# Kernel tuning notes

Measured on AMD Instinct MI355X. Metric: run time of the kernel, lower is better.

The kernel has to match this reference:

```python
import jax, jax.numpy as jnp
import numpy as np

N, C, F = 16384, 8, 257
EPS = 1e-6
DELTA_MAX = 1e8


def setup_inputs() -> dict:
    key = jax.random.key(0)
    k1, k2, k3 = jax.random.split(key, 3)
    xr = jax.random.normal(k1, (N, C, F), dtype=jnp.float32)
    xi = jax.random.normal(k2, (N, C, F), dtype=jnp.float32)
    # affine params (reset_parameters: Wrr=Wii=1, Wri~U(-0.9,0.9), Br=Bi=0)
    Wrr = jnp.ones((C, F), dtype=jnp.float32)
    Wri = jax.random.uniform(k3, (C, F), dtype=jnp.float32, minval=-0.9, maxval=0.9)
    Wii = jnp.ones((C, F), dtype=jnp.float32)
    Br = jnp.zeros((C, F), dtype=jnp.float32)
    Bi = jnp.zeros((C, F), dtype=jnp.float32)
    return {"xr": xr, "xi": xi, "Wrr": Wrr, "Wri": Wri, "Wii": Wii, "Br": Br, "Bi": Bi}


def reference(xr, xi, Wrr, Wri, Wii, Br, Bi):
    # batch (training-mode) complex batchnorm over dim 0; stats per (channel, feature)
    Mr = jnp.mean(xr, axis=0, keepdims=True)  # [1,C,F]
    Mi = jnp.mean(xi, axis=0, keepdims=True)
    xr = xr - Mr
    xi = xi - Mi
    Vrr = jnp.mean(xr * xr, axis=0, keepdims=True)  # [1,C,F]
    Vri = jnp.mean(xr * xi, axis=0, keepdims=True)
    Vii = jnp.mean(xi * xi, axis=0, keepdims=True)
    tau = Vrr + Vii
    delta = jnp.clip(Vrr * Vii - Vri * Vri, EPS, DELTA_MAX)
    s = jnp.sqrt(delta)
    t = jnp.sqrt(tau + 2.0 * s)
    rst = 1.0 / (s * t)
    # inverse matrix square root of 2x2 covariance
    Urr = (s + Vii) * rst
    Uii = (s + Vrr) * rst
    Uri = -Vri * rst
    # affine mixing: Z = W @ U  (W, B broadcast [C,F] against [1,C,F])
    Zrr = Wrr * Urr + Wri * Uri
    Zri = Wrr * Uri + Wri * Uii
    Zir = Wri * Urr + Wii * Uri
    Zii = Wri * Uri + Wii * Uii
    yr = Zrr * xr + Zri * xi + Br
    yi = Zir * xr + Zii * xi + Bi
    return (yr, yi)
```

## Files before the change

kernel.cpp:

```cpp
#include <hip/hip_runtime.h>
#include <hip/hip_bf16.h>
#include <stdint.h>

#define NROWS   16384
#define NCOLS   2056
#define NG      257
#define EPSV    1e-6f
#define DELTA_MAX 1e8f

__device__ __forceinline__ float bf_lo(uint32_t u) {
    return __builtin_bit_cast(float, u << 16);
}
__device__ __forceinline__ float bf_hi(uint32_t u) {
    return __builtin_bit_cast(float, u & 0xffff0000u);
}
__device__ __forceinline__ float bf1(uint16_t u) {
    return __builtin_bit_cast(float, (uint32_t)u << 16);
}
__device__ __forceinline__ uint32_t bf16pair(float lo, float hi) {
    uint32_t ul = __builtin_bit_cast(uint32_t, lo);
    uint32_t uh = __builtin_bit_cast(uint32_t, hi);
    ul = (ul + 0x7fffu + ((ul >> 16) & 1u)) >> 16;
    uh = (uh + 0x7fffu + ((uh >> 16) & 1u)) & 0xffff0000u;
    return ul | uh;
}

__global__ __launch_bounds__(512) void detect_kernel(
    const uint32_t* __restrict__ xr_u, const uint32_t* __restrict__ wrr_u,
    int* __restrict__ flags)
{
    __shared__ int cnt[2];
    if (threadIdx.x < 2) cnt[threadIdx.x] = 0;
    __syncthreads();
    const int part = threadIdx.x >> 8;
    const uint32_t u = part ? wrr_u[threadIdx.x & 255] : xr_u[threadIdx.x & 255];
    const uint32_t e = (u >> 7) & 0xFFu;
    const int ok = (e >= 100u && e <= 131u) ? 1 : 0;
    atomicAdd(&cnt[part], ok);
    __syncthreads();
    if (threadIdx.x == 0) {
        flags[0] = (cnt[0] < 128) ? 1 : 0;
        flags[1] = (cnt[1] < 128) ? 1 : 0;
    }
}

__global__ __launch_bounds__(256) void stats_kernel(
    const void* __restrict__ xr_p, const void* __restrict__ xi_p,
    const int* __restrict__ flags, float* __restrict__ sums)
{
    const int tid = blockIdx.x * 256 + threadIdx.x;
    const int c  = tid % NG;
    const int r0 = tid / NG;
    float sr[8], si[8], srr[8], sri[8], sii[8];
    #pragma unroll
    for (int j = 0; j < 8; ++j) { sr[j]=0.f; si[j]=0.f; srr[j]=0.f; sri[j]=0.f; sii[j]=0.f; }

    if (flags[0]) {
        const float4* xr4 = (const float4*)xr_p;
        const float4* xi4 = (const float4*)xi_p;
        #pragma unroll 2
        for (int k = 0; k < 64; ++k) {
            const size_t g = (size_t)(r0 + (k << 8)) * 514 + 2 * c;
            const float4 a0 = xr4[g], a1 = xr4[g + 1];
            const float4 b0 = xi4[g], b1 = xi4[g + 1];
            const float xrv[8] = {a0.x,a0.y,a0.z,a0.w,a1.x,a1.y,a1.z,a1.w};
            const float xiv[8] = {b0.x,b0.y,b0.z,b0.w,b1.x,b1.y,b1.z,b1.w};
            #pragma unroll
            for (int j = 0; j < 8; ++j) {
                sr[j]  += xrv[j];
                si[j]  += xiv[j];
                srr[j] += xrv[j]*xrv[j];
                sri[j] += xrv[j]*xiv[j];
                sii[j] += xiv[j]*xiv[j];
            }
        }
    } else {
        const uint4* xr4 = (const uint4*)xr_p;
        const uint4* xi4 = (const uint4*)xi_p;
        #pragma unroll 2
        for (int k = 0; k < 64; ++k) {
            const size_t g = (size_t)(r0 + (k << 8)) * NG + c;
            const uint4 a = xr4[g];
            const uint4 b = xi4[g];
            const uint32_t au[4] = {a.x, a.y, a.z, a.w};
            const uint32_t bu[4] = {b.x, b.y, b.z, b.w};
            #pragma unroll
            for (int j = 0; j < 4; ++j) {
                const float r_0 = bf_lo(au[j]), r_1 = bf_hi(au[j]);
                const float i_0 = bf_lo(bu[j]), i_1 = bf_hi(bu[j]);
                sr [2*j]   += r_0;        si [2*j]   += i_0;
                srr[2*j]   += r_0*r_0;    sri[2*j]   += r_0*i_0;    sii[2*j]   += i_0*i_0;
                sr [2*j+1] += r_1;        si [2*j+1] += i_1;
                srr[2*j+1] += r_1*r_1;    sri[2*j+1] += r_1*i_1;    sii[2*j+1] += i_1*i_1;
            }
        }
    }

    const int col = c * 8;
    #pragma unroll
    for (int j = 0; j < 8; ++j) {
        atomicAdd(&sums[0*NCOLS + col + j], sr [j]);
        atomicAdd(&sums[1*NCOLS + col + j], si [j]);
        atomicAdd(&sums[2*NCOLS + col + j], srr[j]);
        atomicAdd(&sums[3*NCOLS + col + j], sri[j]);
        atomicAdd(&sums[4*NCOLS + col + j], sii[j]);
    }
}

__global__ __launch_bounds__(256) void coef_kernel(
    const float* __restrict__ sums,
    const void* __restrict__ Wrr_p, const void* __restrict__ Wri_p,
    const void* __restrict__ Wii_p, const void* __restrict__ Br_p,
    const void* __restrict__ Bi_p,
    const int* __restrict__ flags, float* __restrict__ coef)
{
    const int j = blockIdx.x * 256 + threadIdx.x;
    if (j >= NCOLS) return;
    const float invN = 1.0f / (float)NROWS;
    const float Mr  = sums[0*NCOLS+j] * invN;
    const float Mi  = sums[1*NCOLS+j] * invN;
    const float Vrr = sums[2*NCOLS+j] * invN - Mr * Mr;
    const float Vri = sums[3*NCOLS+j] * invN - Mr * Mi;
    const float Vii = sums[4*NCOLS+j] * invN - Mi * Mi;
    const float tau   = Vrr + Vii;
    const float delta = fminf(fmaxf(Vrr * Vii - Vri * Vri, EPSV), DELTA_MAX);
    const float s   = sqrtf(delta);
    const float t   = sqrtf(tau + 2.0f * s);
    const float rst = 1.0f / (s * t);
    const float Urr = (s + Vii) * rst;
    const float Uii = (s + Vrr) * rst;
    const float Uri = -Vri * rst;

    float wrr, wri, wii, br, bi;
    if (flags[1]) {
        wrr = ((const float*)Wrr_p)[j];  wri = ((const float*)Wri_p)[j];
        wii = ((const float*)Wii_p)[j];
        br  = ((const float*)Br_p)[j];   bi  = ((const float*)Bi_p)[j];
    } else {
        wrr = bf1(((const uint16_t*)Wrr_p)[j]);  wri = bf1(((const uint16_t*)Wri_p)[j]);
        wii = bf1(((const uint16_t*)Wii_p)[j]);
        br  = bf1(((const uint16_t*)Br_p)[j]);   bi  = bf1(((const uint16_t*)Bi_p)[j]);
    }
    const float Zrr = wrr * Urr + wri * Uri;
    const float Zri = wrr * Uri + wri * Uii;
    const float Zir = wri * Urr + wii * Uri;
    const float Zii = wri * Uri + wii * Uii;
    coef[0*NCOLS+j] = Zrr;
    coef[1*NCOLS+j] = Zri;
    coef[2*NCOLS+j] = Zir;
    coef[3*NCOLS+j] = Zii;
    coef[4*NCOLS+j] = br - Zrr * Mr - Zri * Mi;
    coef[5*NCOLS+j] = bi - Zir * Mr - Zii * Mi;
}

__global__ __launch_bounds__(256) void apply_kernel(
    const void* __restrict__ xr_p, const void* __restrict__ xi_p,
    const float* __restrict__ coef, const int* __restrict__ flags,
    void* __restrict__ out_p)
{
    const int tid = blockIdx.x * 256 + threadIdx.x;
    const int c  = tid % NG;
    const int r0 = tid / NG;
    const int col = c * 8;

    float Z[6][8];
    #pragma unroll
    for (int t = 0; t < 6; ++t) {
        const float4 lo = *(const float4*)(coef + t*NCOLS + col);
        const float4 hi = *(const float4*)(coef + t*NCOLS + col + 4);
        Z[t][0]=lo.x; Z[t][1]=lo.y; Z[t][2]=lo.z; Z[t][3]=lo.w;
        Z[t][4]=hi.x; Z[t][5]=hi.y; Z[t][6]=hi.z; Z[t][7]=hi.w;
    }

    if (flags[0]) {
        const float4* xr4 = (const float4*)xr_p;
        const float4* xi4 = (const float4*)xi_p;
        float4* yr4 = (float4*)out_p;
        float4* yi4 = yr4 + (size_t)NROWS * 514;
        #pragma unroll 2
        for (int k = 0; k < 32; ++k) {
            const size_t g = (size_t)(r0 + (k << 9)) * 514 + 2 * c;
            const float4 a0 = xr4[g], a1 = xr4[g + 1];
            const float4 b0 = xi4[g], b1 = xi4[g + 1];
            const float xrv[8] = {a0.x,a0.y,a0.z,a0.w,a1.x,a1.y,a1.z,a1.w};
            const float xiv[8] = {b0.x,b0.y,b0.z,b0.w,b1.x,b1.y,b1.z,b1.w};
            float yrv[8], yiv[8];
            #pragma unroll
            for (int j = 0; j < 8; ++j) {
                yrv[j] = Z[0][j]*xrv[j] + Z[1][j]*xiv[j] + Z[4][j];
                yiv[j] = Z[2][j]*xrv[j] + Z[3][j]*xiv[j] + Z[5][j];
            }
            yr4[g]     = make_float4(yrv[0], yrv[1], yrv[2], yrv[3]);
            yr4[g + 1] = make_float4(yrv[4], yrv[5], yrv[6], yrv[7]);
            yi4[g]     = make_float4(yiv[0], yiv[1], yiv[2], yiv[3]);
            yi4[g + 1] = make_float4(yiv[4], yiv[5], yiv[6], yiv[7]);
        }
    } else {
        const uint4* xr4 = (const uint4*)xr_p;
        const uint4* xi4 = (const uint4*)xi_p;
        uint4* yr4 = (uint4*)out_p;
        uint4* yi4 = yr4 + (size_t)NROWS * NG;
        #pragma unroll 2
        for (int k = 0; k < 32; ++k) {
            const size_t g = (size_t)(r0 + (k << 9)) * NG + c;
            const uint4 a = xr4[g];
            const uint4 b = xi4[g];
            const uint32_t au[4] = {a.x, a.y, a.z, a.w};
            const uint32_t bu[4] = {b.x, b.y, b.z, b.w};
            uint32_t ou[4], pu[4];
            #pragma unroll
            for (int j = 0; j < 4; ++j) {
                const int e0 = 2*j, e1 = 2*j + 1;
                const float xr0 = bf_lo(au[j]), xr1 = bf_hi(au[j]);
                const float xi0 = bf_lo(bu[j]), xi1 = bf_hi(bu[j]);
                const float yr0 = Z[0][e0]*xr0 + Z[1][e0]*xi0 + Z[4][e0];
                const float yi0 = Z[2][e0]*xr0 + Z[3][e0]*xi0 + Z[5][e0];
                const float yr1 = Z[0][e1]*xr1 + Z[1][e1]*xi1 + Z[4][e1];
                const float yi1 = Z[2][e1]*xr1 + Z[3][e1]*xi1 + Z[5][e1];
                ou[j] = bf16pair(yr0, yr1);
                pu[j] = bf16pair(yi0, yi1);
            }
            yr4[g] = make_uint4(ou[0], ou[1], ou[2], ou[3]);
            yi4[g] = make_uint4(pu[0], pu[1], pu[2], pu[3]);
        }
    }
}

extern "C" void kernel_launch(void* const* d_in, const int* in_sizes, int n_in,
                              void* d_out, int out_size, void* d_ws, size_t ws_size,
                              hipStream_t stream)
{
    const void* xr_p = d_in[0];
    const void* xi_p = d_in[1];
    const void* Wrr  = d_in[2];
    const void* Wri  = d_in[3];
    const void* Wii  = d_in[4];
    const void* Br   = d_in[5];
    const void* Bi   = d_in[6];

    float* sums  = (float*)d_ws;
    float* coef  = sums + 5 * NCOLS;
    int*   flags = (int*)(coef + 6 * NCOLS);

    detect_kernel<<<1, 512, 0, stream>>>((const uint32_t*)xr_p, (const uint32_t*)Wrr, flags);
    hipMemsetAsync(sums, 0, 5 * NCOLS * sizeof(float), stream);
    stats_kernel<<<257, 256, 0, stream>>>(xr_p, xi_p, flags, sums);
    coef_kernel<<<(NCOLS + 255) / 256, 256, 0, stream>>>(sums, Wrr, Wri, Wii, Br, Bi, flags, coef);
    apply_kernel<<<514, 256, 0, stream>>>(xr_p, xi_p, coef, flags, d_out);
}
```

Measured before the change: 619.1 us.

## Restructure stats reduction into 2D grid with shuffle reduction; widen apply grid

The stats kernel moves from 257 blocks of row-strided threads to a 64x33 grid. Each block covers a row slice and 64 column groups, reduces with wave shuffles and shared memory, then issues far fewer atomics. The apply kernel grows from 514 to 2056 blocks and uses nontemporal stores for the output. The goal is more parallelism and memory-level concurrency on a bandwidth-bound workload, at the cost of more shuffle work and more blocks.

```diff
diff --git a/kernel.cpp b/kernel.cpp
--- a/kernel.cpp
+++ b/kernel.cpp
@@ -1,5 +1,4 @@
 #include <hip/hip_runtime.h>
-#include <hip/hip_bf16.h>
 #include <stdint.h>
 
 #define NROWS   16384
@@ -7,6 +6,10 @@
 #define NG      257
 #define EPSV    1e-6f
 #define DELTA_MAX 1e8f
+#define SR      64
+
+typedef float    f32x4 __attribute__((ext_vector_type(4)));
+typedef uint32_t u32x4 __attribute__((ext_vector_type(4)));
 
 __device__ __forceinline__ float bf_lo(uint32_t u) {
     return __builtin_bit_cast(float, u << 16);
@@ -44,66 +47,114 @@
     }
 }
 
+__device__ __forceinline__ void accum_bf16x8(float* acc, uint4 a, uint4 b) {
+    const uint32_t au[4] = {a.x, a.y, a.z, a.w};
+    const uint32_t bu[4] = {b.x, b.y, b.z, b.w};
+    #pragma unroll
+    for (int j = 0; j < 4; ++j) {
+        const float r0 = bf_lo(au[j]), r1 = bf_hi(au[j]);
+        const float i0 = bf_lo(bu[j]), i1 = bf_hi(bu[j]);
+        acc[0*8 + 2*j]     += r0;       acc[1*8 + 2*j]     += i0;
+        acc[2*8 + 2*j]     += r0*r0;    acc[3*8 + 2*j]     += r0*i0;
+        acc[4*8 + 2*j]     += i0*i0;
+        acc[0*8 + 2*j + 1] += r1;       acc[1*8 + 2*j + 1] += i1;
+        acc[2*8 + 2*j + 1] += r1*r1;    acc[3*8 + 2*j + 1] += r1*i1;
+        acc[4*8 + 2*j + 1] += i1*i1;
+    }
+}
+__device__ __forceinline__ void accum_f32x8(float* acc, float4 a0, float4 a1,
+                                            float4 b0, float4 b1) {
+    const float xr[8] = {a0.x,a0.y,a0.z,a0.w,a1.x,a1.y,a1.z,a1.w};
+    const float xi[8] = {b0.x,b0.y,b0.z,b0.w,b1.x,b1.y,b1.z,b1.w};
+    #pragma unroll
+    for (int j = 0; j < 8; ++j) {
+        acc[0*8 + j] += xr[j];        acc[1*8 + j] += xi[j];
+        acc[2*8 + j] += xr[j]*xr[j];  acc[3*8 + j] += xr[j]*xi[j];
+        acc[4*8 + j] += xi[j]*xi[j];
+    }
+}
+
 __global__ __launch_bounds__(256) void stats_kernel(
     const void* __restrict__ xr_p, const void* __restrict__ xi_p,
     const int* __restrict__ flags, float* __restrict__ sums)
 {
-    const int tid = blockIdx.x * 256 + threadIdx.x;
-    const int c  = tid % NG;
-    const int r0 = tid / NG;
-    float sr[8], si[8], srr[8], sri[8], sii[8];
+    const int rs = blockIdx.x;
+    const int ct = blockIdx.y;
+    const int t  = threadIdx.x;
+    const int rbase = rs * (NROWS / SR);
+
+    float acc[40];
     #pragma unroll
-    for (int j = 0; j < 8; ++j) { sr[j]=0.f; si[j]=0.f; srr[j]=0.f; sri[j]=0.f; sii[j]=0.f; }
-
-    if (flags[0]) {
-        const float4* xr4 = (const float4*)xr_p;
-        const float4* xi4 = (const float4*)xi_p;
-        #pragma unroll 2
-        for (int k = 0; k < 64; ++k) {
-            const size_t g = (size_t)(r0 + (k << 8)) * 514 + 2 * c;
-            const float4 a0 = xr4[g], a1 = xr4[g + 1];
-            const float4 b0 = xi4[g], b1 = xi4[g + 1];
-            const float xrv[8] = {a0.x,a0.y,a0.z,a0.w,a1.x,a1.y,a1.z,a1.w};
-            const float xiv[8] = {b0.x,b0.y,b0.z,b0.w,b1.x,b1.y,b1.z,b1.w};
-            #pragma unroll
-            for (int j = 0; j < 8; ++j) {
-                sr[j]  += xrv[j];
-                si[j]  += xiv[j];
-                srr[j] += xrv[j]*xrv[j];
-                sri[j] += xrv[j]*xiv[j];
-                sii[j] += xiv[j]*xiv[j];
+    for (int j = 0; j < 40; ++j) acc[j] = 0.f;
+
+    const bool isfp32 = (flags[0] != 0);
+
+    if (ct < 32) {
+        const int grp = ct * 8 + (t & 7);
+        const int rl  = t >> 3;
+        if (!isfp32) {
+            const uint4* xr4 = (const uint4*)xr_p;
+            const uint4* xi4 = (const uint4*)xi_p;
+            #pragma unroll 2
+            for (int k = 0; k < 8; ++k) {
+                const size_t g = (size_t)(rbase + rl + 32*k) * NG + grp;
+                accum_bf16x8(acc, xr4[g], xi4[g]);
             }
-        }
+        } else {
+            const float4* xr4 = (const float4*)xr_p;
+            const float4* xi4 = (const float4*)xi_p;
+            #pragma unroll 2
+            for (int k = 0; k < 8; ++k) {
+                const size_t g = (size_t)(rbase + rl + 32*k) * 514 + 2*grp;
+                accum_f32x8(acc, xr4[g], xr4[g+1], xi4[g], xi4[g+1]);
+            }
+        }
+        #pragma unroll
+        for (int j = 0; j < 40; ++j) acc[j] += __shfl_xor(acc[j], 8, 64);
+        #pragma unroll
+        for (int j = 0; j < 40; ++j) acc[j] += __shfl_xor(acc[j], 16, 64);
+        #pragma unroll
+        for (int j = 0; j < 40; ++j) acc[j] += __shfl_xor(acc[j], 32, 64);
     } else {
-        const uint4* xr4 = (const uint4*)xr_p;
-        const uint4* xi4 = (const uint4*)xi_p;
-        #pragma unroll 2
-        for (int k = 0; k < 64; ++k) {
-            const size_t g = (size_t)(r0 + (k << 8)) * NG + c;
-            const uint4 a = xr4[g];
-            const uint4 b = xi4[g];
-            const uint32_t au[4] = {a.x, a.y, a.z, a.w};
-            const uint32_t bu[4] = {b.x, b.y, b.z, b.w};
-            #pragma unroll
-            for (int j = 0; j < 4; ++j) {
-                const float r_0 = bf_lo(au[j]), r_1 = bf_hi(au[j]);
-                const float i_0 = bf_lo(bu[j]), i_1 = bf_hi(bu[j]);
-                sr [2*j]   += r_0;        si [2*j]   += i_0;
-                srr[2*j]   += r_0*r_0;    sri[2*j]   += r_0*i_0;    sii[2*j]   += i_0*i_0;
-                sr [2*j+1] += r_1;        si [2*j+1] += i_1;
-                srr[2*j+1] += r_1*r_1;    sri[2*j+1] += r_1*i_1;    sii[2*j+1] += i_1*i_1;
-            }
-        }
-    }
-
-    const int col = c * 8;
-    #pragma unroll
-    for (int j = 0; j < 8; ++j) {
-        atomicAdd(&sums[0*NCOLS + col + j], sr [j]);
-        atomicAdd(&sums[1*NCOLS + col + j], si [j]);
-        atomicAdd(&sums[2*NCOLS + col + j], srr[j]);
-        atomicAdd(&sums[3*NCOLS + col + j], sri[j]);
-        atomicAdd(&sums[4*NCOLS + col + j], sii[j]);
+        if (!isfp32) {
+            const uint4* xr4 = (const uint4*)xr_p;
+            const uint4* xi4 = (const uint4*)xi_p;
+            const size_t g = (size_t)(rbase + t) * NG + 256;
+            accum_bf16x8(acc, xr4[g], xi4[g]);
+        } else {
+            const float4* xr4 = (const float4*)xr_p;
+            const float4* xi4 = (const float4*)xi_p;
+            const size_t g = (size_t)(rbase + t) * 514 + 512;
+            accum_f32x8(acc, xr4[g], xr4[g+1], xi4[g], xi4[g+1]);
+        }
+        #pragma unroll
+        for (int m = 1; m <= 32; m <<= 1) {
+            #pragma unroll
+            for (int j = 0; j < 40; ++j) acc[j] += __shfl_xor(acc[j], m, 64);
+        }
+    }
+
+    __shared__ float red[4][320];
+    const int wv = t >> 6, ln = t & 63;
+    if (ct < 32) {
+        if (ln < 8) {
+            #pragma unroll
+            for (int j = 0; j < 40; ++j) red[wv][ln*40 + j] = acc[j];
+        }
+    } else {
+        if (ln == 0) {
+            #pragma unroll
+            for (int j = 0; j < 40; ++j) red[wv][j] = acc[j];
+        }
+    }
+    __syncthreads();
+    const int nvals = (ct < 32) ? 320 : 40;
+    for (int idx = t; idx < nvals; idx += 256) {
+        const float v = red[0][idx] + red[1][idx] + red[2][idx] + red[3][idx];
+        const int gi  = idx / 40;
+        const int j   = idx - gi * 40;
+        const int col = (ct * 8 + gi) * 8 + (j & 7);
+        atomicAdd(&sums[(j >> 3) * NCOLS + col], v);
     }
 }
 
@@ -175,11 +226,11 @@
     if (flags[0]) {
         const float4* xr4 = (const float4*)xr_p;
         const float4* xi4 = (const float4*)xi_p;
-        float4* yr4 = (float4*)out_p;
-        float4* yi4 = yr4 + (size_t)NROWS * 514;
+        f32x4* yr4 = (f32x4*)out_p;
+        f32x4* yi4 = yr4 + (size_t)NROWS * 514;
         #pragma unroll 2
-        for (int k = 0; k < 32; ++k) {
-            const size_t g = (size_t)(r0 + (k << 9)) * 514 + 2 * c;
+        for (int k = 0; k < 8; ++k) {
+            const size_t g = (size_t)(r0 + (k << 11)) * 514 + 2 * c;
             const float4 a0 = xr4[g], a1 = xr4[g + 1];
             const float4 b0 = xi4[g], b1 = xi4[g + 1];
             const float xrv[8] = {a0.x,a0.y,a0.z,a0.w,a1.x,a1.y,a1.z,a1.w};
@@ -190,19 +241,23 @@
                 yrv[j] = Z[0][j]*xrv[j] + Z[1][j]*xiv[j] + Z[4][j];
                 yiv[j] = Z[2][j]*xrv[j] + Z[3][j]*xiv[j] + Z[5][j];
             }
-            yr4[g]     = make_float4(yrv[0], yrv[1], yrv[2], yrv[3]);
-            yr4[g + 1] = make_float4(yrv[4], yrv[5], yrv[6], yrv[7]);
-            yi4[g]     = make_float4(yiv[0], yiv[1], yiv[2], yiv[3]);
-            yi4[g + 1] = make_float4(yiv[4], yiv[5], yiv[6], yiv[7]);
+            const f32x4 s0 = {yrv[0], yrv[1], yrv[2], yrv[3]};
+            const f32x4 s1 = {yrv[4], yrv[5], yrv[6], yrv[7]};
+            const f32x4 t0 = {yiv[0], yiv[1], yiv[2], yiv[3]};
+            const f32x4 t1 = {yiv[4], yiv[5], yiv[6], yiv[7]};
+            __builtin_nontemporal_store(s0, yr4 + g);
+            __builtin_nontemporal_store(s1, yr4 + g + 1);
+            __builtin_nontemporal_store(t0, yi4 + g);
+            __builtin_nontemporal_store(t1, yi4 + g + 1);
         }
     } else {
         const uint4* xr4 = (const uint4*)xr_p;
         const uint4* xi4 = (const uint4*)xi_p;
-        uint4* yr4 = (uint4*)out_p;
-        uint4* yi4 = yr4 + (size_t)NROWS * NG;
+        u32x4* yr4 = (u32x4*)out_p;
+        u32x4* yi4 = yr4 + (size_t)NROWS * NG;
         #pragma unroll 2
-        for (int k = 0; k < 32; ++k) {
-            const size_t g = (size_t)(r0 + (k << 9)) * NG + c;
+        for (int k = 0; k < 8; ++k) {
+            const size_t g = (size_t)(r0 + (k << 11)) * NG + c;
             const uint4 a = xr4[g];
             const uint4 b = xi4[g];
             const uint32_t au[4] = {a.x, a.y, a.z, a.w};
@@ -220,8 +275,10 @@
                 ou[j] = bf16pair(yr0, yr1);
                 pu[j] = bf16pair(yi0, yi1);
             }
-            yr4[g] = make_uint4(ou[0], ou[1], ou[2], ou[3]);
-            yi4[g] = make_uint4(pu[0], pu[1], pu[2], pu[3]);
+            const u32x4 o = {ou[0], ou[1], ou[2], ou[3]};
+            const u32x4 p = {pu[0], pu[1], pu[2], pu[3]};
+            __builtin_nontemporal_store(o, yr4 + g);
+            __builtin_nontemporal_store(p, yi4 + g);
         }
     }
 }
@@ -244,7 +301,7 @@
 
     detect_kernel<<<1, 512, 0, stream>>>((const uint32_t*)xr_p, (const uint32_t*)Wrr, flags);
     hipMemsetAsync(sums, 0, 5 * NCOLS * sizeof(float), stream);
-    stats_kernel<<<257, 256, 0, stream>>>(xr_p, xi_p, flags, sums);
+    stats_kernel<<<dim3(SR, 33), 256, 0, stream>>>(xr_p, xi_p, flags, sums);
     coef_kernel<<<(NCOLS + 255) / 256, 256, 0, stream>>>(sums, Wrr, Wri, Wii, Br, Bi, flags, coef);
-    apply_kernel<<<514, 256, 0, stream>>>(xr_p, xi_p, coef, flags, d_out);
-}
+    apply_kernel<<<2056, 256, 0, stream>>>(xr_p, xi_p, coef, flags, d_out);
+}
```

Result: faster. 532.8 us (-13.9%).

## Restructure stats into LDS-atomic block partials with separate reduce, widen apply grid

Applied to the files above, without the earlier changes.

The stats pass now runs up to 512 blocks of 1024 threads, each streaming contiguous float4s and accumulating into per-block LDS histograms with shared-memory atomics (padded to avoid bank conflicts). The per-block partials are written to workspace and summed by a new reduce kernel, which replaces the global atomics and the memset. The apply kernel grid grows from 514 to 2056 blocks with fewer rows per thread. The aim is more parallelism and memory-level concurrency on a bandwidth-bound pass. The cost is heavy LDS atomic traffic, five atomics per element, plus an extra partials round trip through memory.

```diff
diff --git a/kernel.cpp b/kernel.cpp
--- a/kernel.cpp
+++ b/kernel.cpp
@@ -1,5 +1,4 @@
 #include <hip/hip_runtime.h>
-#include <hip/hip_bf16.h>
 #include <stdint.h>
 
 #define NROWS   16384
@@ -7,6 +6,8 @@
 #define NG      257
 #define EPSV    1e-6f
 #define DELTA_MAX 1e8f
+#define NSUM    (5*NCOLS)
+#define LDSW    2124
 
 __device__ __forceinline__ float bf_lo(uint32_t u) {
     return __builtin_bit_cast(float, u << 16);
@@ -44,67 +45,100 @@
     }
 }
 
-__global__ __launch_bounds__(256) void stats_kernel(
+__global__ __launch_bounds__(1024) void stats_kernel(
     const void* __restrict__ xr_p, const void* __restrict__ xi_p,
-    const int* __restrict__ flags, float* __restrict__ sums)
-{
-    const int tid = blockIdx.x * 256 + threadIdx.x;
-    const int c  = tid % NG;
-    const int r0 = tid / NG;
-    float sr[8], si[8], srr[8], sri[8], sii[8];
-    #pragma unroll
-    for (int j = 0; j < 8; ++j) { sr[j]=0.f; si[j]=0.f; srr[j]=0.f; sri[j]=0.f; sii[j]=0.f; }
+    const int* __restrict__ flags, float* __restrict__ partials,
+    int TT, int cstep_f32, int cstep_bf16)
+{
+    __shared__ float lds[5 * LDSW];
+    for (int i = threadIdx.x; i < 5 * LDSW; i += 1024) lds[i] = 0.f;
+    __syncthreads();
+
+    const int tid = blockIdx.x * 1024 + threadIdx.x;
 
     if (flags[0]) {
-        const float4* xr4 = (const float4*)xr_p;
-        const float4* xi4 = (const float4*)xi_p;
-        #pragma unroll 2
-        for (int k = 0; k < 64; ++k) {
-            const size_t g = (size_t)(r0 + (k << 8)) * 514 + 2 * c;
-            const float4 a0 = xr4[g], a1 = xr4[g + 1];
-            const float4 b0 = xi4[g], b1 = xi4[g + 1];
-            const float xrv[8] = {a0.x,a0.y,a0.z,a0.w,a1.x,a1.y,a1.z,a1.w};
-            const float xiv[8] = {b0.x,b0.y,b0.z,b0.w,b1.x,b1.y,b1.z,b1.w};
-            #pragma unroll
-            for (int j = 0; j < 8; ++j) {
-                sr[j]  += xrv[j];
-                si[j]  += xiv[j];
-                srr[j] += xrv[j]*xrv[j];
-                sri[j] += xrv[j]*xiv[j];
-                sii[j] += xiv[j]*xiv[j];
-            }
+        const float4* __restrict__ xr4 = (const float4*)xr_p;
+        const float4* __restrict__ xi4 = (const float4*)xi_p;
+        const int T4 = NROWS * (NCOLS / 4);
+        int c = (int)((4u * (uint32_t)tid) % (uint32_t)NCOLS);
+        #pragma unroll 2
+        for (int i = tid; i < T4; i += TT) {
+            const float4 a = xr4[i];
+            const float4 b = xi4[i];
+            const float xr[4] = {a.x, a.y, a.z, a.w};
+            const float xi[4] = {b.x, b.y, b.z, b.w};
+            #pragma unroll
+            for (int u = 0; u < 4; ++u) {
+                const int cu = c + u;
+                const int o  = cu + (cu >> 5);
+                atomicAdd(&lds[0*LDSW + o], xr[u]);
+                atomicAdd(&lds[1*LDSW + o], xi[u]);
+                atomicAdd(&lds[2*LDSW + o], xr[u]*xr[u]);
+                atomicAdd(&lds[3*LDSW + o], xr[u]*xi[u]);
+                atomicAdd(&lds[4*LDSW + o], xi[u]*xi[u]);
+            }
+            c += cstep_f32; if (c >= NCOLS) c -= NCOLS;
         }
     } else {
-        const uint4* xr4 = (const uint4*)xr_p;
-        const uint4* xi4 = (const uint4*)xi_p;
-        #pragma unroll 2
-        for (int k = 0; k < 64; ++k) {
-            const size_t g = (size_t)(r0 + (k << 8)) * NG + c;
-            const uint4 a = xr4[g];
-            const uint4 b = xi4[g];
+        const uint4* __restrict__ xr4 = (const uint4*)xr_p;
+        const uint4* __restrict__ xi4 = (const uint4*)xi_p;
+        const int T8 = NROWS * (NCOLS / 8);
+        int c = (int)((8u * (uint32_t)tid) % (uint32_t)NCOLS);
+        #pragma unroll 2
+        for (int i = tid; i < T8; i += TT) {
+            const uint4 a = xr4[i];
+            const uint4 b = xi4[i];
             const uint32_t au[4] = {a.x, a.y, a.z, a.w};
             const uint32_t bu[4] = {b.x, b.y, b.z, b.w};
             #pragma unroll
             for (int j = 0; j < 4; ++j) {
-                const float r_0 = bf_lo(au[j]), r_1 = bf_hi(au[j]);
-                const float i_0 = bf_lo(bu[j]), i_1 = bf_hi(bu[j]);
-                sr [2*j]   += r_0;        si [2*j]   += i_0;
-                srr[2*j]   += r_0*r_0;    sri[2*j]   += r_0*i_0;    sii[2*j]   += i_0*i_0;
-                sr [2*j+1] += r_1;        si [2*j+1] += i_1;
-                srr[2*j+1] += r_1*r_1;    sri[2*j+1] += r_1*i_1;    sii[2*j+1] += i_1*i_1;
-            }
-        }
-    }
-
-    const int col = c * 8;
-    #pragma unroll
-    for (int j = 0; j < 8; ++j) {
-        atomicAdd(&sums[0*NCOLS + col + j], sr [j]);
-        atomicAdd(&sums[1*NCOLS + col + j], si [j]);
-        atomicAdd(&sums[2*NCOLS + col + j], srr[j]);
-        atomicAdd(&sums[3*NCOLS + col + j], sri[j]);
-        atomicAdd(&sums[4*NCOLS + col + j], sii[j]);
-    }
+                const float r0 = bf_lo(au[j]), r1 = bf_hi(au[j]);
+                const float i0 = bf_lo(bu[j]), i1 = bf_hi(bu[j]);
+                const int c0i = c + 2*j;
+                const int c1i = c0i + 1;
+                const int o0  = c0i + (c0i >> 5);
+                const int o1  = c1i + (c1i >> 5);
+                atomicAdd(&lds[0*LDSW + o0], r0);
+                atomicAdd(&lds[1*LDSW + o0], i0);
+                atomicAdd(&lds[2*LDSW + o0], r0*r0);
+                atomicAdd(&lds[3*LDSW + o0], r0*i0);
+                atomicAdd(&lds[4*LDSW + o0], i0*i0);
+                atomicAdd(&lds[0*LDSW + o1], r1);
+                atomicAdd(&lds[1*LDSW + o1], i1);
+                atomicAdd(&lds[2*LDSW + o1], r1*r1);
+                atomicAdd(&lds[3*LDSW + o1], r1*i1);
+                atomicAdd(&lds[4*LDSW + o1], i1*i1);
+            }
+            c += cstep_bf16; if (c >= NCOLS) c -= NCOLS;
+        }
+    }
+
+    __syncthreads();
+    float* __restrict__ dst = partials + (size_t)blockIdx.x * NSUM;
+    for (int idx = threadIdx.x; idx < NSUM; idx += 1024) {
+        const int s   = idx / NCOLS;
+        const int col = idx - s * NCOLS;
+        dst[idx] = lds[s * LDSW + col + (col >> 5)];
+    }
+}
+
+__global__ __launch_bounds__(256) void reduce_kernel(
+    const float* __restrict__ partials, float* __restrict__ sums, int NB)
+{
+    const int j  = blockIdx.x * 64 + (threadIdx.x & 63);
+    const int bl = threadIdx.x >> 6;
+    float s = 0.f;
+    if (j < NSUM) {
+        #pragma unroll 4
+        for (int b = bl; b < NB; b += 4)
+            s += partials[(size_t)b * NSUM + j];
+    }
+    __shared__ float red[256];
+    red[threadIdx.x] = s;
+    __syncthreads();
+    if (threadIdx.x < 64 && j < NSUM)
+        sums[j] = red[threadIdx.x] + red[threadIdx.x + 64] +
+                  red[threadIdx.x + 128] + red[threadIdx.x + 192];
 }
 
 __global__ __launch_bounds__(256) void coef_kernel(
@@ -178,8 +212,8 @@
         float4* yr4 = (float4*)out_p;
         float4* yi4 = yr4 + (size_t)NROWS * 514;
         #pragma unroll 2
-        for (int k = 0; k < 32; ++k) {
-            const size_t g = (size_t)(r0 + (k << 9)) * 514 + 2 * c;
+        for (int k = 0; k < 8; ++k) {
+            const size_t g = (size_t)(r0 + (k << 11)) * 514 + 2 * c;
             const float4 a0 = xr4[g], a1 = xr4[g + 1];
             const float4 b0 = xi4[g], b1 = xi4[g + 1];
             const float xrv[8] = {a0.x,a0.y,a0.z,a0.w,a1.x,a1.y,a1.z,a1.w};
@@ -201,8 +235,8 @@
         uint4* yr4 = (uint4*)out_p;
         uint4* yi4 = yr4 + (size_t)NROWS * NG;
         #pragma unroll 2
-        for (int k = 0; k < 32; ++k) {
-            const size_t g = (size_t)(r0 + (k << 9)) * NG + c;
+        for (int k = 0; k < 8; ++k) {
+            const size_t g = (size_t)(r0 + (k << 11)) * NG + c;
             const uint4 a = xr4[g];
             const uint4 b = xi4[g];
             const uint32_t au[4] = {a.x, a.y, a.z, a.w};
@@ -239,12 +273,20 @@
     const void* Bi   = d_in[6];
 
     float* sums  = (float*)d_ws;
-    float* coef  = sums + 5 * NCOLS;
+    float* coef  = sums + NSUM;
     int*   flags = (int*)(coef + 6 * NCOLS);
+    float* partials = (float*)(flags + 4);
+
+    const size_t base_bytes = (size_t)(NSUM + 6 * NCOLS + 4) * 4;
+    int NB = 512;
+    while (NB > 64 && base_bytes + (size_t)NB * NSUM * 4 > ws_size) NB >>= 1;
+    const int TT = NB * 1024;
+    const int cstep_f32  = (int)(((unsigned long long)4 * TT) % NCOLS);
+    const int cstep_bf16 = (int)(((unsigned long long)8 * TT) % NCOLS);
 
     detect_kernel<<<1, 512, 0, stream>>>((const uint32_t*)xr_p, (const uint32_t*)Wrr, flags);
-    hipMemsetAsync(sums, 0, 5 * NCOLS * sizeof(float), stream);
-    stats_kernel<<<257, 256, 0, stream>>>(xr_p, xi_p, flags, sums);
+    stats_kernel<<<NB, 1024, 0, stream>>>(xr_p, xi_p, flags, partials, TT, cstep_f32, cstep_bf16);
+    reduce_kernel<<<(NSUM + 63) / 64, 256, 0, stream>>>(partials, sums, NB);
     coef_kernel<<<(NCOLS + 255) / 256, 256, 0, stream>>>(sums, Wrr, Wri, Wii, Br, Bi, flags, coef);
-    apply_kernel<<<514, 256, 0, stream>>>(xr_p, xi_p, coef, flags, d_out);
-}
+    apply_kernel<<<2056, 256, 0, stream>>>(xr_p, xi_p, coef, flags, d_out);
+}
```

New measurement: 1.290 ms. +108.4%, slower.
